# Kernel tuning notes

Measured on AMD Instinct MI355X. Metric: run time of the kernel, lower is better.

The kernel has to match this reference:

```python
import jax, jax.numpy as jnp
import numpy as np

N_NODES = 100000
N_EDGES = 3200000
F_IN = 256
D_OUT = 64
BATCH = 4096
N_FIELDS = 20


def setup_inputs() -> dict:
    key = jax.random.key(0)
    k1, k2, k3, k4 = jax.random.split(key, 4)
    features = jax.random.normal(k1, (N_NODES, F_IN), dtype=jnp.float32)
    edge_index = jax.random.randint(k2, (2, N_EDGES), 0, N_NODES, dtype=jnp.int32)
    W = jax.random.normal(k3, (F_IN, D_OUT), dtype=jnp.float32) * 0.05
    b = jnp.zeros((D_OUT,), dtype=jnp.float32)
    x = jax.random.randint(k4, (BATCH, N_FIELDS), 0, N_NODES, dtype=jnp.int32)
    return {"features": features, "edge_index": edge_index, "W": W, "b": b, "x": x}


def reference(features, edge_index, W, b, x):
    # PyG GCNConv: add self-loops, symmetric normalization, linear transform,
    # scatter-add aggregation, then final index by x.
    n = features.shape[0]
    loop = jnp.arange(n, dtype=edge_index.dtype)
    src = jnp.concatenate([edge_index[0], loop])  # [E+N]
    dst = jnp.concatenate([edge_index[1], loop])
    ones = jnp.ones(src.shape[0], dtype=features.dtype)
    deg = jax.ops.segment_sum(ones, dst, num_segments=n)  # in-degree incl. self-loop
    deg_inv_sqrt = jnp.where(deg > 0, jax.lax.rsqrt(deg), 0.0)
    norm = deg_inv_sqrt[src] * deg_inv_sqrt[dst]  # [E+N]
    xw = features @ W  # [N, D] -- transform before aggregation (fewer FLOPs)
    msg = xw[src] * norm[:, None]  # gather + scale
    out = jax.ops.segment_sum(msg, dst, num_segments=n) + b  # [N, D]
    return out[x]  # [batch, num_fields, D]
```

## Files before the change

### kernel.cpp

```cpp
#include <hip/hip_runtime.h>
#include <hip/hip_bf16.h>

#define N_NODES 100000
#define N_EDGES 3200000
#define F_IN 256
#define D_OUT 64
#define BATCH 4096
#define N_FIELDS 20
#define N_ENTRIES (BATCH * N_FIELDS)

#define NBUCKET 512
#define NPB 196
#define N_PAD (NBUCKET * NPB)
#define EPB 16384
#define NBLK ((N_EDGES + EPB - 1) / EPB)
#define BUCKET_CAP 8192
#define SCAN_B 512
#define NSB (N_PAD / SCAN_B)
#define CNT_BLKS (N_ENTRIES / 256)
#define GEMM_BLKS ((N_NODES + 63) / 64)

typedef short bf16x8 __attribute__((ext_vector_type(8)));
typedef float f32x4 __attribute__((ext_vector_type(4)));

static __device__ __forceinline__ unsigned short f2bf_bits(float x) {
    __hip_bfloat16 h = __float2bfloat16(x);
    return *reinterpret_cast<unsigned short*>(&h);
}

__global__ void k_wtconv(const float* __restrict__ W, unsigned short* __restrict__ WTbf) {
    int i = blockIdx.x * blockDim.x + threadIdx.x;
    if (i >= D_OUT * F_IN) return;
    int n = i >> 8, k = i & 255;
    WTbf[i] = f2bf_bits(W[k * D_OUT + n]);
}

__global__ __launch_bounds__(256) void k_front(const uint4* __restrict__ dst4,
                                               unsigned short* __restrict__ perBlockCnt,
                                               const int* __restrict__ x,
                                               int* __restrict__ nodeEntCnt,
                                               unsigned* __restrict__ refBits,
                                               const float* __restrict__ feat,
                                               const unsigned short* __restrict__ WTbf,
                                               float* __restrict__ yf) {
    __shared__ unsigned hist[NBUCKET];
    __shared__ unsigned short wt[64 * 264];
    int tid = threadIdx.x;

    if (blockIdx.x < NBLK) {
        hist[tid] = 0;
        hist[tid + 256] = 0;
        __syncthreads();
        int base4 = blockIdx.x * (EPB / 4);
#pragma unroll
        for (int k = 0; k < EPB / 1024; k++) {
            int e4 = base4 + k * 256 + tid;
            if (e4 < N_EDGES / 4) {
                uint4 d = dst4[e4];
                atomicAdd(&hist[d.x / NPB], 1u);
                atomicAdd(&hist[d.y / NPB], 1u);
                atomicAdd(&hist[d.z / NPB], 1u);
                atomicAdd(&hist[d.w / NPB], 1u);
            }
        }
        __syncthreads();
        perBlockCnt[(tid) * NBLK + blockIdx.x] = (unsigned short)hist[tid];
        perBlockCnt[(tid + 256) * NBLK + blockIdx.x] = (unsigned short)hist[tid + 256];
    } else if (blockIdx.x < NBLK + CNT_BLKS) {
        int ent = (blockIdx.x - NBLK) * 256 + tid;
        if (ent < N_ENTRIES) {
            int node = x[ent];
            atomicAdd(&nodeEntCnt[node], 1);
            atomicOr(&refBits[node >> 5], 1u << (node & 31));
        }
    } else {
        int gb = blockIdx.x - NBLK - CNT_BLKS;
        {
            int r = tid >> 2, seg = tid & 3;
            const uint4* gsrc = (const uint4*)(WTbf + r * 256 + seg * 64);
            uint4* ldst = (uint4*)&wt[r * 264 + seg * 64];
#pragma unroll
            for (int q = 0; q < 8; q++) ldst[q] = gsrc[q];
        }
        __syncthreads();

        int wave = tid >> 6, lane = tid & 63;
        int quad = lane >> 4, m = lane & 15;
        int rowT = gb * 64 + wave * 16;
        int row = rowT + m;
        int rowC = (row < N_NODES) ? row : (N_NODES - 1);
        const float* fb = feat + (size_t)rowC * F_IN + quad * 8;

        f32x4 acc0 = {0.f, 0.f, 0.f, 0.f};
        f32x4 acc1 = acc0, acc2 = acc0, acc3 = acc0;

#pragma unroll
        for (int kk = 0; kk < 8; kk++) {
            float4 x0 = *(const float4*)(fb + kk * 32);
            float4 x1 = *(const float4*)(fb + kk * 32 + 4);
            bf16x8 a;
            a[0] = (short)f2bf_bits(x0.x); a[1] = (short)f2bf_bits(x0.y);
            a[2] = (short)f2bf_bits(x0.z); a[3] = (short)f2bf_bits(x0.w);
            a[4] = (short)f2bf_bits(x1.x); a[5] = (short)f2bf_bits(x1.y);
            a[6] = (short)f2bf_bits(x1.z); a[7] = (short)f2bf_bits(x1.w);
            int kbase = kk * 32 + quad * 8;
            bf16x8 b0 = *(const bf16x8*)&wt[(0 * 16 + m) * 264 + kbase];
            bf16x8 b1 = *(const bf16x8*)&wt[(1 * 16 + m) * 264 + kbase];
            bf16x8 b2 = *(const bf16x8*)&wt[(2 * 16 + m) * 264 + kbase];
            bf16x8 b3 = *(const bf16x8*)&wt[(3 * 16 + m) * 264 + kbase];
            acc0 = __builtin_amdgcn_mfma_f32_16x16x32_bf16(a, b0, acc0, 0, 0, 0);
            acc1 = __builtin_amdgcn_mfma_f32_16x16x32_bf16(a, b1, acc1, 0, 0, 0);
            acc2 = __builtin_amdgcn_mfma_f32_16x16x32_bf16(a, b2, acc2, 0, 0, 0);
            acc3 = __builtin_amdgcn_mfma_f32_16x16x32_bf16(a, b3, acc3, 0, 0, 0);
        }

#pragma unroll
        for (int r = 0; r < 4; r++) {
            int rr = rowT + quad * 4 + r;
            if (rr < N_NODES) {
                size_t o = (size_t)rr * D_OUT + m;
                yf[o]      = acc0[r];
                yf[o + 16] = acc1[r];
                yf[o + 32] = acc2[r];
                yf[o + 48] = acc3[r];
            }
        }
    }
}

__global__ __launch_bounds__(512) void k_scans(const int* __restrict__ nodeEntCnt,
                                               int* __restrict__ localE,
                                               int* __restrict__ blockSumsE,
                                               unsigned short* __restrict__ perBlockCnt,
                                               int* __restrict__ bucketTot) {
    if (blockIdx.x < NSB) {
        __shared__ int sh[SCAN_B];
        int g = blockIdx.x * SCAN_B + threadIdx.x;
        int v = (g < N_PAD) ? nodeEntCnt[g] : 0;
        sh[threadIdx.x] = v;
        __syncthreads();
        for (int off = 1; off < SCAN_B; off <<= 1) {
            int t = (threadIdx.x >= off) ? sh[threadIdx.x - off] : 0;
            __syncthreads();
            sh[threadIdx.x] += t;
            __syncthreads();
        }
        int incl = sh[threadIdx.x];
        if (g < N_PAD) localE[g] = incl - v;
        if (threadIdx.x == SCAN_B - 1) blockSumsE[blockIdx.x] = incl;
    } else {
        int gw = ((blockIdx.x - NSB) * 512 + threadIdx.x) >> 6;
        int lane = threadIdx.x & 63;
        if (gw >= NBUCKET) return;
        unsigned running = 0;
        for (int c = 0; c < (NBLK + 63) / 64; c++) {
            int blk = c * 64 + lane;
            int idx = gw * NBLK + blk;
            unsigned v = (blk < NBLK) ? perBlockCnt[idx] : 0;
            unsigned orig = v;
#pragma unroll
            for (int d = 1; d < 64; d <<= 1) {
                unsigned t = __shfl_up(v, d, 64);
                if (lane >= d) v += t;
            }
            if (blk < NBLK) perBlockCnt[idx] = (unsigned short)(running + v - orig);
            running += __shfl(v, 63, 64);
        }
        if (lane == 0) bucketTot[gw] = (int)running;
    }
}

__global__ __launch_bounds__(512) void k_base2(const int* __restrict__ bucketTot,
                                               int* __restrict__ bucketBase,
                                               const int* __restrict__ blockSumsE,
                                               int* __restrict__ blockBaseE) {
    __shared__ int sh[512];
    int tid = threadIdx.x;
    if (blockIdx.x == 0) {
        int v = bucketTot[tid];
        sh[tid] = v;
        __syncthreads();
        for (int off = 1; off < 512; off <<= 1) {
            int t = (tid >= off) ? sh[tid - off] : 0;
            __syncthreads();
            sh[tid] += t;
            __syncthreads();
        }
        bucketBase[tid] = sh[tid] - v;
        if (tid == NBUCKET - 1) bucketBase[NBUCKET] = sh[NBUCKET - 1];
    } else {
        int v = (tid < NSB) ? blockSumsE[tid] : 0;
        sh[tid] = v;
        __syncthreads();
        for (int off = 1; off < 512; off <<= 1) {
            int t = (tid >= off) ? sh[tid - off] : 0;
            __syncthreads();
            sh[tid] += t;
            __syncthreads();
        }
        if (tid < NSB) blockBaseE[tid] = sh[tid] - v;
    }
}

__global__ __launch_bounds__(256) void k_scatters(const uint4* __restrict__ src4,
                                                  const uint4* __restrict__ dst4,
                                                  const int* __restrict__ bucketBase,
                                                  const unsigned short* __restrict__ perBlockCnt,
                                                  unsigned* __restrict__ bucketData,
                                                  const int* __restrict__ x,
                                                  int* __restrict__ localE,
                                                  const int* __restrict__ blockBaseE,
                                                  int* __restrict__ entGrouped) {
    if (blockIdx.x < NBLK) {
        __shared__ unsigned slotBase[NBUCKET];
        slotBase[threadIdx.x] = (unsigned)bucketBase[threadIdx.x] +
                                (unsigned)perBlockCnt[threadIdx.x * NBLK + blockIdx.x];
        slotBase[threadIdx.x + 256] = (unsigned)bucketBase[threadIdx.x + 256] +
                                      (unsigned)perBlockCnt[(threadIdx.x + 256) * NBLK + blockIdx.x];
        __syncthreads();
        int base4 = blockIdx.x * (EPB / 4);
#pragma unroll
        for (int k = 0; k < EPB / 1024; k++) {
            int e4 = base4 + k * 256 + threadIdx.x;
            if (e4 < N_EDGES / 4) {
                uint4 s = src4[e4];
                uint4 d = dst4[e4];
                unsigned ss[4] = {s.x, s.y, s.z, s.w};
                unsigned dd[4] = {d.x, d.y, d.z, d.w};
#pragma unroll
                for (int j = 0; j < 4; j++) {
                    unsigned b = dd[j] / NPB;
                    unsigned ld = dd[j] - b * NPB;
                    unsigned slot = atomicAdd(&slotBase[b], 1u);
                    bucketData[slot] = ss[j] | (ld << 17);
                }
            }
        }
    } else {
        int ent = (blockIdx.x - NBLK) * 256 + threadIdx.x;
        if (ent < N_ENTRIES) {
            int node = x[ent];
            int posL = atomicAdd(&localE[node], 1);
            entGrouped[blockBaseE[node >> 9] + posL] = ent;
        }
    }
}

__global__ __launch_bounds__(256) void k_bucket_csr(unsigned* __restrict__ bucketData,
                                                    const int* __restrict__ bucketBase,
                                                    const unsigned* __restrict__ refBits,
                                                    int* __restrict__ rowStart,
                                                    unsigned short* __restrict__ deg,
                                                    const float* __restrict__ yf,
                                                    unsigned short* __restrict__ y) {
    __shared__ unsigned srcsorted[BUCKET_CAP];
    __shared__ unsigned nodeCount[NPB];
    __shared__ unsigned sscan[256];
    __shared__ unsigned cursor[NPB];
    __shared__ unsigned char refF[NPB];

    int b = blockIdx.x;
    int base = bucketBase[b];
    int cnt = bucketBase[b + 1] - base;
    if (cnt > BUCKET_CAP) cnt = BUCKET_CAP;
    int tid = threadIdx.x;

    for (int j = tid; j < NPB; j += 256) nodeCount[j] = 0;
    __syncthreads();

    for (int i = tid; i < cnt; i += 256) {
        unsigned w = bucketData[base + i];
        atomicAdd(&nodeCount[w >> 17], 1u);
    }
    __syncthreads();

    int firstNode = b * NPB;
    unsigned refCnt = 0;
    if (tid < NPB) {
        int node = firstNode + tid;
        unsigned isRef = (refBits[node >> 5] >> (node & 31)) & 1u;
        refF[tid] = (unsigned char)isRef;
        refCnt = isRef ? nodeCount[tid] : 0;
        deg[node] = (unsigned short)nodeCount[tid];
    }
    sscan[tid] = refCnt;
    __syncthreads();
    for (int off = 1; off < 256; off <<= 1) {
        unsigned t = (tid >= off) ? sscan[tid - off] : 0;
        __syncthreads();
        sscan[tid] += t;
        __syncthreads();
    }

    if (tid < NPB) {
        unsigned excl = sscan[tid] - refCnt;
        rowStart[firstNode + tid] = base + (int)excl;
        cursor[tid] = excl;
    }
    __syncthreads();

    for (int i = tid; i < cnt; i += 256) {
        unsigned w = bucketData[base + i];
        unsigned ld = w >> 17;
        if (refF[ld]) {
            unsigned slot = atomicAdd(&cursor[ld], 1u);
            srcsorted[slot] = w & 0x1FFFFu;
        }
    }
    __syncthreads();

    int refTotal = (int)sscan[255];
    for (int i = tid; i < refTotal; i += 256)
        bucketData[base + i] = srcsorted[i];

    for (int idx = tid; idx < NPB * 16; idx += 256) {
        int j = idx >> 4;
        int node = firstNode + j;
        if (node < N_NODES) {
            float ds = rsqrtf((float)nodeCount[j] + 1.0f);
            float4 v = ((const float4*)(yf + (size_t)node * D_OUT))[idx & 15];
            uint2 pw;
            pw.x = (unsigned)f2bf_bits(v.x * ds) | ((unsigned)f2bf_bits(v.y * ds) << 16);
            pw.y = (unsigned)f2bf_bits(v.z * ds) | ((unsigned)f2bf_bits(v.w * ds) << 16);
            ((uint2*)(y + (size_t)node * D_OUT))[idx & 15] = pw;
        }
    }
}

static __device__ __forceinline__ void acc4(f32x4& a, uint2 v, float msk) {
    a[0] += msk * __uint_as_float(v.x << 16);
    a[1] += msk * __uint_as_float(v.x & 0xffff0000u);
    a[2] += msk * __uint_as_float(v.y << 16);
    a[3] += msk * __uint_as_float(v.y & 0xffff0000u);
}

__global__ __launch_bounds__(256) void k_agg(const int* __restrict__ entGrouped,
                                             const int* __restrict__ localE,
                                             const int* __restrict__ blockBaseE,
                                             const int* __restrict__ rowStart,
                                             const unsigned short* __restrict__ deg,
                                             const unsigned* __restrict__ sortedSrc,
                                             const unsigned short* __restrict__ y,
                                             const float* __restrict__ b,
                                             float* __restrict__ out) {
    int g = blockIdx.x * blockDim.x + threadIdx.x;
    int i = g >> 6, lane = g & 63;
    if (i >= N_PAD) return;
    int gEnd = blockBaseE[i >> 9] + localE[i];
    int gStart = (i == 0) ? 0 : (blockBaseE[(i - 1) >> 9] + localE[i - 1]);
    int cntEnt = gEnd - gStart;
    if (cntEnt <= 0) return;

    int grp = lane >> 4;
    int m = lane & 15;
    int start = rowStart[i];
    int cnt = deg[i];
    float disI = rsqrtf((float)(cnt + 1));

    uint2 sv = *(const uint2*)(y + ((unsigned)i << 6) + (m << 2));

    f32x4 a0 = {0.f, 0.f, 0.f, 0.f};
    f32x4 a1 = a0, a2 = a0, a3 = a0;

    for (int e = 0; e < cnt; e += 32) {
        int e0 = e + grp,      e1 = e + 4 + grp,  e2 = e + 8 + grp,  e3 = e + 12 + grp;
        int e4 = e + 16 + grp, e5 = e + 20 + grp, e6 = e + 24 + grp, e7 = e + 28 + grp;
        unsigned r0 = (e0 < cnt) ? sortedSrc[start + e0] : (unsigned)i;
        unsigned r1 = (e1 < cnt) ? sortedSrc[start + e1] : (unsigned)i;
        unsigned r2 = (e2 < cnt) ? sortedSrc[start + e2] : (unsigned)i;
        unsigned r3 = (e3 < cnt) ? sortedSrc[start + e3] : (unsigned)i;
        unsigned r4 = (e4 < cnt) ? sortedSrc[start + e4] : (unsigned)i;
        unsigned r5 = (e5 < cnt) ? sortedSrc[start + e5] : (unsigned)i;
        unsigned r6 = (e6 < cnt) ? sortedSrc[start + e6] : (unsigned)i;
        unsigned r7 = (e7 < cnt) ? sortedSrc[start + e7] : (unsigned)i;
        uint2 v0 = *(const uint2*)(y + (r0 << 6) + (m << 2));
        uint2 v1 = *(const uint2*)(y + (r1 << 6) + (m << 2));
        uint2 v2 = *(const uint2*)(y + (r2 << 6) + (m << 2));
        uint2 v3 = *(const uint2*)(y + (r3 << 6) + (m << 2));
        uint2 v4 = *(const uint2*)(y + (r4 << 6) + (m << 2));
        uint2 v5 = *(const uint2*)(y + (r5 << 6) + (m << 2));
        uint2 v6 = *(const uint2*)(y + (r6 << 6) + (m << 2));
        uint2 v7 = *(const uint2*)(y + (r7 << 6) + (m << 2));
        acc4(a0, v0, (e0 < cnt) ? 1.f : 0.f);
        acc4(a1, v1, (e1 < cnt) ? 1.f : 0.f);
        acc4(a2, v2, (e2 < cnt) ? 1.f : 0.f);
        acc4(a3, v3, (e3 < cnt) ? 1.f : 0.f);
        acc4(a0, v4, (e4 < cnt) ? 1.f : 0.f);
        acc4(a1, v5, (e5 < cnt) ? 1.f : 0.f);
        acc4(a2, v6, (e6 < cnt) ? 1.f : 0.f);
        acc4(a3, v7, (e7 < cnt) ? 1.f : 0.f);
    }

    f32x4 s;
#pragma unroll
    for (int c = 0; c < 4; c++) s[c] = (a0[c] + a1[c]) + (a2[c] + a3[c]);
#pragma unroll
    for (int c = 0; c < 4; c++) {
        s[c] += __shfl_xor(s[c], 16, 64);
        s[c] += __shfl_xor(s[c], 32, 64);
    }

    float4 b4 = *(const float4*)(b + (m << 2));
    float4 val;
    val.x = disI * (s[0] + __uint_as_float(sv.x << 16)) + b4.x;
    val.y = disI * (s[1] + __uint_as_float(sv.x & 0xffff0000u)) + b4.y;
    val.z = disI * (s[2] + __uint_as_float(sv.y << 16)) + b4.z;
    val.w = disI * (s[3] + __uint_as_float(sv.y & 0xffff0000u)) + b4.w;

    for (int j = grp; j < cntEnt; j += 4) {
        int ent = entGrouped[gStart + j];
        *(float4*)(out + (size_t)ent * D_OUT + (m << 2)) = val;
    }
}

extern "C" void kernel_launch(void* const* d_in, const int* in_sizes, int n_in,
                              void* d_out, int out_size, void* d_ws, size_t ws_size,
                              hipStream_t stream) {
    const float* feat     = (const float*)d_in[0];
    const int* edge_index = (const int*)d_in[1];
    const float* W        = (const float*)d_in[2];
    const float* bsrc     = (const float*)d_in[3];
    const int* x          = (const int*)d_in[4];
    float* out            = (float*)d_out;

    const uint4* src4 = (const uint4*)edge_index;
    const uint4* dst4 = (const uint4*)(edge_index + N_EDGES);

    char* ws = (char*)d_ws;
    size_t off = 0;
    auto alloc = [&](size_t bytes) {
        size_t o = off;
        off = (off + bytes + 255) & ~(size_t)255;
        return o;
    };
    int* bucketBase = (int*)(ws + alloc((size_t)(NBUCKET + 1) * 4));
    int* bucketTot  = (int*)(ws + alloc((size_t)NBUCKET * 4));
    size_t ecOff = alloc((size_t)N_PAD * 4);
    int* nodeEntCnt = (int*)(ws + ecOff);
    int* entGrouped = (int*)(ws + ecOff);
    unsigned* refBits = (unsigned*)(ws + alloc((size_t)(N_PAD / 8)));
    size_t rsOff = alloc((size_t)N_PAD * 4);
    unsigned short* perBlockCnt = (unsigned short*)(ws + rsOff);
    int* rowStart   = (int*)(ws + rsOff);
    unsigned short* deg = (unsigned short*)(ws + alloc((size_t)N_PAD * 2));
    unsigned short* WTbf = (unsigned short*)(ws + alloc((size_t)D_OUT * F_IN * 2));
    int* localE     = (int*)(ws + alloc((size_t)N_PAD * 4));
    int* blockSumsE = (int*)(ws + alloc((size_t)NSB * 4));
    int* blockBaseE = (int*)(ws + alloc((size_t)NSB * 4));
    unsigned* bucketData = (unsigned*)(ws + alloc((size_t)N_EDGES * 4));
    unsigned short* y = (unsigned short*)(ws + alloc((size_t)N_NODES * D_OUT * 2));
    float* yf       = (float*)(ws + alloc((size_t)N_NODES * D_OUT * 4));
    (void)ws_size; (void)in_sizes; (void)n_in; (void)out_size;

    const int T = 256;
    (void)hipMemsetAsync(nodeEntCnt, 0, (size_t)N_PAD * 4, stream);
    (void)hipMemsetAsync(refBits, 0, (size_t)(N_PAD / 8), stream);
    k_wtconv<<<(D_OUT * F_IN + T - 1) / T, T, 0, stream>>>(W, WTbf);
    k_front<<<NBLK + CNT_BLKS + GEMM_BLKS, T, 0, stream>>>(dst4, perBlockCnt, x, nodeEntCnt,
                                                           refBits, feat, WTbf, yf);
    k_scans<<<NSB + 64, 512, 0, stream>>>(nodeEntCnt, localE, blockSumsE, perBlockCnt, bucketTot);
    k_base2<<<2, 512, 0, stream>>>(bucketTot, bucketBase, blockSumsE, blockBaseE);
    k_scatters<<<NBLK + CNT_BLKS, T, 0, stream>>>(src4, dst4, bucketBase, perBlockCnt, bucketData,
                                                  x, localE, blockBaseE, entGrouped);
    k_bucket_csr<<<NBUCKET, T, 0, stream>>>(bucketData, bucketBase, refBits, rowStart, deg, yf, y);
    k_agg<<<((size_t)N_PAD * 64 + T - 1) / T, T, 0, stream>>>(
        entGrouped, localE, blockBaseE, rowStart, deg, bucketData, y, bsrc, out);
}
```

Baseline: 318.4 us.

## Stage edge scatter through shared-memory local sort and coalesce GEMM feature loads

The edge scatter kernel now recomputes a per-block bucket histogram, scans it, and sorts the block's edges into shared memory by bucket. It then writes them out contiguously per bucket, found by binary search, so the global writes to bucketData are grouped instead of scattered one word at a time. Separately, the GEMM branch stages the feature tile through shared memory as bf16 in two K halves, so global reads are row-contiguous float4 loads. The cost is a second pass over dst, an extra scan and barriers, 64KB of shared memory per scatter block (which lowers occupancy), and an extra LDS round trip in the GEMM.

```diff
diff --git a/kernel.cpp b/kernel.cpp
--- a/kernel.cpp
+++ b/kernel.cpp
@@ -45,6 +45,7 @@
                                                float* __restrict__ yf) {
     __shared__ unsigned hist[NBUCKET];
     __shared__ unsigned short wt[64 * 264];
+    __shared__ unsigned short at[64 * 136];
     int tid = threadIdx.x;
 
     if (blockIdx.x < NBLK) {
@@ -82,36 +83,44 @@
 #pragma unroll
             for (int q = 0; q < 8; q++) ldst[q] = gsrc[q];
         }
-        __syncthreads();
 
         int wave = tid >> 6, lane = tid & 63;
         int quad = lane >> 4, m = lane & 15;
-        int rowT = gb * 64 + wave * 16;
-        int row = rowT + m;
-        int rowC = (row < N_NODES) ? row : (N_NODES - 1);
-        const float* fb = feat + (size_t)rowC * F_IN + quad * 8;
+        int rowBase = gb * 64;
+        int rowT = rowBase + wave * 16;
 
         f32x4 acc0 = {0.f, 0.f, 0.f, 0.f};
         f32x4 acc1 = acc0, acc2 = acc0, acc3 = acc0;
 
-#pragma unroll
-        for (int kk = 0; kk < 8; kk++) {
-            float4 x0 = *(const float4*)(fb + kk * 32);
-            float4 x1 = *(const float4*)(fb + kk * 32 + 4);
-            bf16x8 a;
-            a[0] = (short)f2bf_bits(x0.x); a[1] = (short)f2bf_bits(x0.y);
-            a[2] = (short)f2bf_bits(x0.z); a[3] = (short)f2bf_bits(x0.w);
-            a[4] = (short)f2bf_bits(x1.x); a[5] = (short)f2bf_bits(x1.y);
-            a[6] = (short)f2bf_bits(x1.z); a[7] = (short)f2bf_bits(x1.w);
-            int kbase = kk * 32 + quad * 8;
-            bf16x8 b0 = *(const bf16x8*)&wt[(0 * 16 + m) * 264 + kbase];
-            bf16x8 b1 = *(const bf16x8*)&wt[(1 * 16 + m) * 264 + kbase];
-            bf16x8 b2 = *(const bf16x8*)&wt[(2 * 16 + m) * 264 + kbase];
-            bf16x8 b3 = *(const bf16x8*)&wt[(3 * 16 + m) * 264 + kbase];
-            acc0 = __builtin_amdgcn_mfma_f32_16x16x32_bf16(a, b0, acc0, 0, 0, 0);
-            acc1 = __builtin_amdgcn_mfma_f32_16x16x32_bf16(a, b1, acc1, 0, 0, 0);
-            acc2 = __builtin_amdgcn_mfma_f32_16x16x32_bf16(a, b2, acc2, 0, 0, 0);
-            acc3 = __builtin_amdgcn_mfma_f32_16x16x32_bf16(a, b3, acc3, 0, 0, 0);
+        for (int kh = 0; kh < 2; ++kh) {
+            if (kh) __syncthreads();
+#pragma unroll
+            for (int it = 0; it < 8; ++it) {
+                int f = it * 1024 + tid * 4;
+                int r = f >> 7, c = f & 127;
+                int rr = rowBase + r;
+                int rc = (rr < N_NODES) ? rr : (N_NODES - 1);
+                float4 v = *(const float4*)(feat + (size_t)rc * F_IN + kh * 128 + c);
+                uint2 pw;
+                pw.x = (unsigned)f2bf_bits(v.x) | ((unsigned)f2bf_bits(v.y) << 16);
+                pw.y = (unsigned)f2bf_bits(v.z) | ((unsigned)f2bf_bits(v.w) << 16);
+                *(uint2*)&at[r * 136 + c] = pw;
+            }
+            __syncthreads();
+#pragma unroll
+            for (int k2 = 0; k2 < 4; ++k2) {
+                int kb = k2 * 32 + quad * 8;
+                int kbase = kh * 128 + kb;
+                bf16x8 a = *(const bf16x8*)&at[(wave * 16 + m) * 136 + kb];
+                bf16x8 b0 = *(const bf16x8*)&wt[(0 * 16 + m) * 264 + kbase];
+                bf16x8 b1 = *(const bf16x8*)&wt[(1 * 16 + m) * 264 + kbase];
+                bf16x8 b2 = *(const bf16x8*)&wt[(2 * 16 + m) * 264 + kbase];
+                bf16x8 b3 = *(const bf16x8*)&wt[(3 * 16 + m) * 264 + kbase];
+                acc0 = __builtin_amdgcn_mfma_f32_16x16x32_bf16(a, b0, acc0, 0, 0, 0);
+                acc1 = __builtin_amdgcn_mfma_f32_16x16x32_bf16(a, b1, acc1, 0, 0, 0);
+                acc2 = __builtin_amdgcn_mfma_f32_16x16x32_bf16(a, b2, acc2, 0, 0, 0);
+                acc3 = __builtin_amdgcn_mfma_f32_16x16x32_bf16(a, b3, acc3, 0, 0, 0);
+            }
         }
 
 #pragma unroll
@@ -211,17 +220,58 @@
                                                   int* __restrict__ localE,
                                                   const int* __restrict__ blockBaseE,
                                                   int* __restrict__ entGrouped) {
+    __shared__ unsigned sortbuf[EPB];
+    __shared__ int lbE[NBUCKET + 1];
+    __shared__ unsigned cur[NBUCKET];
+    __shared__ unsigned sbG[NBUCKET];
+    int tid = threadIdx.x;
+
     if (blockIdx.x < NBLK) {
-        __shared__ unsigned slotBase[NBUCKET];
-        slotBase[threadIdx.x] = (unsigned)bucketBase[threadIdx.x] +
-                                (unsigned)perBlockCnt[threadIdx.x * NBLK + blockIdx.x];
-        slotBase[threadIdx.x + 256] = (unsigned)bucketBase[threadIdx.x + 256] +
-                                      (unsigned)perBlockCnt[(threadIdx.x + 256) * NBLK + blockIdx.x];
-        __syncthreads();
-        int base4 = blockIdx.x * (EPB / 4);
+        int blk = blockIdx.x;
+        sbG[tid] = (unsigned)bucketBase[tid] +
+                   (unsigned)perBlockCnt[tid * NBLK + blk];
+        sbG[tid + 256] = (unsigned)bucketBase[tid + 256] +
+                         (unsigned)perBlockCnt[(tid + 256) * NBLK + blk];
+        cur[tid] = 0;
+        cur[tid + 256] = 0;
+        __syncthreads();
+
+        int base4 = blk * (EPB / 4);
 #pragma unroll
         for (int k = 0; k < EPB / 1024; k++) {
-            int e4 = base4 + k * 256 + threadIdx.x;
+            int e4 = base4 + k * 256 + tid;
+            if (e4 < N_EDGES / 4) {
+                uint4 d = dst4[e4];
+                atomicAdd(&cur[d.x / NPB], 1u);
+                atomicAdd(&cur[d.y / NPB], 1u);
+                atomicAdd(&cur[d.z / NPB], 1u);
+                atomicAdd(&cur[d.w / NPB], 1u);
+            }
+        }
+        __syncthreads();
+        unsigned c0 = cur[tid], c1 = cur[tid + 256];
+        lbE[tid] = (int)c0;
+        lbE[tid + 256] = (int)c1;
+        __syncthreads();
+        for (int off = 1; off < 512; off <<= 1) {
+            int t0 = (tid >= off) ? lbE[tid - off] : 0;
+            int t1 = lbE[tid + 256 - off];
+            __syncthreads();
+            lbE[tid] += t0;
+            lbE[tid + 256] += t1;
+            __syncthreads();
+        }
+        int incl0 = lbE[tid], incl1 = lbE[tid + 256];
+        __syncthreads();
+        lbE[tid] = incl0 - (int)c0;
+        lbE[tid + 256] = incl1 - (int)c1;
+        cur[tid] = (unsigned)(incl0 - (int)c0);
+        cur[tid + 256] = (unsigned)(incl1 - (int)c1);
+        if (tid == 255) lbE[NBUCKET] = incl1;
+        __syncthreads();
+#pragma unroll
+        for (int k = 0; k < EPB / 1024; k++) {
+            int e4 = base4 + k * 256 + tid;
             if (e4 < N_EDGES / 4) {
                 uint4 s = src4[e4];
                 uint4 d = dst4[e4];
@@ -231,13 +281,24 @@
                 for (int j = 0; j < 4; j++) {
                     unsigned b = dd[j] / NPB;
                     unsigned ld = dd[j] - b * NPB;
-                    unsigned slot = atomicAdd(&slotBase[b], 1u);
-                    bucketData[slot] = ss[j] | (ld << 17);
+                    unsigned slot = atomicAdd(&cur[b], 1u);
+                    sortbuf[slot] = ss[j] | (ld << 17);
                 }
             }
         }
+        __syncthreads();
+        int ecnt = lbE[NBUCKET];
+        for (int i = tid; i < ecnt; i += 256) {
+            unsigned w = sortbuf[i];
+            int lo = 0, hi = NBUCKET;
+            while (hi - lo > 1) {
+                int mid = (lo + hi) >> 1;
+                if (lbE[mid] <= i) lo = mid; else hi = mid;
+            }
+            bucketData[sbG[lo] + (unsigned)(i - lbE[lo])] = w;
+        }
     } else {
-        int ent = (blockIdx.x - NBLK) * 256 + threadIdx.x;
+        int ent = (blockIdx.x - NBLK) * 256 + tid;
         if (ent < N_ENTRIES) {
             int node = x[ent];
             int posL = atomicAdd(&localE[node], 1);
```

Result: slower. 336.3 us (+5.6%).
